# Optimization experiments

Measured on AMD Instinct MI355X. Metric: run time of the kernel, lower is better.

## Reference

```python
import jax, jax.numpy as jnp
import numpy as np
from functools import partial

B, C, H, W = 64, 3, 64, 64
D = 64            # hidden_dim == slot dim
S = 7             # num_slots
ITERS = 3
EPS_ATTN = 1e-8
MLP_HID = 128     # max(dim, 128)


def conv5_same(x, w, b):
    # x: [B, Cin, H, W], w: [Cout, Cin, 5, 5]
    y = jax.lax.conv_general_dilated(
        x, w, window_strides=(1, 1), padding='SAME',
        dimension_numbers=('NCHW', 'OIHW', 'NCHW'))
    return y + b[None, :, None, None]


def layernorm(x, w, b, eps):
    mu = jnp.mean(x, axis=-1, keepdims=True)
    var = jnp.var(x, axis=-1, keepdims=True)
    return (x - mu) * jax.lax.rsqrt(var + eps) * w + b


def build_grid(h, w):
    rr = jnp.linspace(0.0, 1.0, h)
    cc = jnp.linspace(0.0, 1.0, w)
    g = jnp.stack(jnp.meshgrid(rr, cc, indexing='ij'), axis=-1)  # [H,W,2]
    return jnp.concatenate([g, 1.0 - g], axis=-1)                # [H,W,4]


def setup_inputs() -> dict:
    key = jax.random.key(0)
    ks = jax.random.split(key, 32)
    sc = lambda fan: 1.0 / np.sqrt(fan)
    inp = {
        'image': jax.random.normal(ks[0], (B, C, H, W), jnp.float32),
        'slots_noise': jax.random.normal(ks[1], (B, S, D), jnp.float32),
        'conv0_w': jax.random.normal(ks[2], (D, 3, 5, 5), jnp.float32) * sc(3 * 25),
        'conv0_b': jnp.zeros((D,), jnp.float32),
        'conv1_w': jax.random.normal(ks[3], (D, D, 5, 5), jnp.float32) * sc(D * 25),
        'conv1_b': jnp.zeros((D,), jnp.float32),
        'conv2_w': jax.random.normal(ks[4], (D, D, 5, 5), jnp.float32) * sc(D * 25),
        'conv2_b': jnp.zeros((D,), jnp.float32),
        'conv3_w': jax.random.normal(ks[5], (D, D, 5, 5), jnp.float32) * sc(D * 25),
        'conv3_b': jnp.zeros((D,), jnp.float32),
        'pos_w': jax.random.normal(ks[6], (D, 4), jnp.float32) * sc(4),
        'pos_b': jnp.zeros((D,), jnp.float32),
        'fc1_w': jax.random.normal(ks[7], (D, D), jnp.float32) * sc(D),
        'fc1_b': jnp.zeros((D,), jnp.float32),
        'fc2_w': jax.random.normal(ks[8], (D, D), jnp.float32) * sc(D),
        'fc2_b': jnp.zeros((D,), jnp.float32),
        'slots_mu': jax.random.uniform(ks[9], (1, 1, D), jnp.float32, -0.3, 0.3),
        'slots_log_sigma': jax.random.uniform(ks[10], (1, 1, D), jnp.float32, -0.3, 0.3),
        'q_w': jax.random.normal(ks[11], (D, D), jnp.float32) * sc(D),
        'k_w': jax.random.normal(ks[12], (D, D), jnp.float32) * sc(D),
        'v_w': jax.random.normal(ks[13], (D, D), jnp.float32) * sc(D),
        'gru_w_ih': jax.random.normal(ks[14], (3 * D, D), jnp.float32) * sc(D),
        'gru_w_hh': jax.random.normal(ks[15], (3 * D, D), jnp.float32) * sc(D),
        'gru_b_ih': jnp.zeros((3 * D,), jnp.float32),
        'gru_b_hh': jnp.zeros((3 * D,), jnp.float32),
        'mlp1_w': jax.random.normal(ks[16], (MLP_HID, D), jnp.float32) * sc(D),
        'mlp1_b': jnp.zeros((MLP_HID,), jnp.float32),
        'mlp2_w': jax.random.normal(ks[17], (D, MLP_HID), jnp.float32) * sc(MLP_HID),
        'mlp2_b': jnp.zeros((D,), jnp.float32),
        'ln_in_w': jnp.ones((D,), jnp.float32),
        'ln_in_b': jnp.zeros((D,), jnp.float32),
        'ln_slots_w': jnp.ones((D,), jnp.float32),
        'ln_slots_b': jnp.zeros((D,), jnp.float32),
        'ln_ff_w': jnp.ones((D,), jnp.float32),
        'ln_ff_b': jnp.zeros((D,), jnp.float32),
    }
    return inp


def reference(image, slots_noise, conv0_w, conv0_b, conv1_w, conv1_b,
              conv2_w, conv2_b, conv3_w, conv3_b, pos_w, pos_b,
              fc1_w, fc1_b, fc2_w, fc2_b, slots_mu, slots_log_sigma,
              q_w, k_w, v_w, gru_w_ih, gru_w_hh, gru_b_ih, gru_b_hh,
              mlp1_w, mlp1_b, mlp2_w, mlp2_b,
              ln_in_w, ln_in_b, ln_slots_w, ln_slots_b, ln_ff_w, ln_ff_b):
    b = image.shape[0]
    # --- CNN encoder ---
    x = jax.nn.relu(conv5_same(image, conv0_w, conv0_b))
    x = jax.nn.relu(conv5_same(x, conv1_w, conv1_b))
    x = jax.nn.relu(conv5_same(x, conv2_w, conv2_b))
    x = jax.nn.relu(conv5_same(x, conv3_w, conv3_b))
    x = jnp.transpose(x, (0, 2, 3, 1))                 # [B,H,W,D]
    pos = build_grid(x.shape[1], x.shape[2]) @ pos_w.T + pos_b
    x = x + pos[None]
    x = x.reshape(b, -1, D)                            # [B,N,D]
    # LayerNorm over (N, D) jointly, fresh affine (w=1, b=0), eps=1e-5
    mu = jnp.mean(x, axis=(1, 2), keepdims=True)
    var = jnp.var(x, axis=(1, 2), keepdims=True)
    x = (x - mu) * jax.lax.rsqrt(var + 1e-5)
    # --- fc MLP ---
    x = jax.nn.relu(x @ fc1_w.T + fc1_b) @ fc2_w.T + fc2_b
    # --- Slot attention ---
    scale = D ** (-0.5)
    slots = slots_mu + jnp.exp(slots_log_sigma) * slots_noise  # [B,S,D]
    inp = layernorm(x, ln_in_w, ln_in_b, 1e-3)
    k = inp @ k_w.T                                    # [B,N,D]
    v = inp @ v_w.T
    for _ in range(ITERS):
        slots_prev = slots
        q = layernorm(slots, ln_slots_w, ln_slots_b, 1e-3) @ q_w.T  # [B,S,D]
        dots = jnp.einsum('bid,bjd->bij', q, k) * scale             # [B,S,N]
        attn = jax.nn.softmax(dots, axis=1) + EPS_ATTN              # over slots
        attn = attn / jnp.sum(attn, axis=-1, keepdims=True)
        updates = jnp.einsum('bjd,bij->bid', v, attn)               # [B,S,D]
        # GRUCell(updates, slots_prev)
        gi = updates @ gru_w_ih.T + gru_b_ih                        # [B,S,3D]
        gh = slots_prev @ gru_w_hh.T + gru_b_hh
        i_r, i_z, i_n = jnp.split(gi, 3, axis=-1)
        h_r, h_z, h_n = jnp.split(gh, 3, axis=-1)
        r = jax.nn.sigmoid(i_r + h_r)
        z = jax.nn.sigmoid(i_z + h_z)
        n = jnp.tanh(i_n + r * h_n)
        slots = (1.0 - z) * n + z * slots_prev
        # residual MLP
        h = layernorm(slots, ln_ff_w, ln_ff_b, 1e-3)
        slots = slots + (jax.nn.relu(h @ mlp1_w.T + mlp1_b) @ mlp2_w.T + mlp2_b)
    return slots
```

## Files before the change

### kernel.cpp

```cpp
#include <hip/hip_runtime.h>

#define HW 64
#define BATCH 64
#define DDIM 64
#define NSLOT 7
#define NPOS 4096

typedef __attribute__((ext_vector_type(8))) short short8;
typedef __attribute__((ext_vector_type(4))) short short4v;
typedef __attribute__((ext_vector_type(4))) float floatx4;

__device__ __forceinline__ float wave_sum(float x) {
  #pragma unroll
  for (int o = 32; o >= 1; o >>= 1) x += __shfl_xor(x, o, 64);
  return x;
}

__device__ __forceinline__ unsigned short f2bf(float f) {
  unsigned int u = __float_as_uint(f);
  return (unsigned short)((u + 0x7fffu + ((u >> 16) & 1u)) >> 16);
}
__device__ __forceinline__ float bf2f(unsigned short u) {
  return __uint_as_float(((unsigned int)u) << 16);
}
__device__ __forceinline__ short4v pack4(float a, float b, float c, float d) {
  short4v s;
  s.x = (short)f2bf(a); s.y = (short)f2bf(b);
  s.z = (short)f2bf(c); s.w = (short)f2bf(d);
  return s;
}

__global__ __launch_bounds__(256) void prep_w(
    const float* __restrict__ w1, const float* __restrict__ w2,
    const float* __restrict__ w3, unsigned short* __restrict__ wp)
{
  int idx = blockIdx.x * 256 + threadIdx.x;
  if (idx >= 3 * 102400) return;
  int L = idx / 102400;
  int rem = idx - L * 102400;
  int tap = rem >> 12;
  int r2  = rem & 4095;
  int ks = r2 >> 11;
  int mt = (r2 >> 9) & 3;
  int l  = (r2 >> 3) & 63;
  int j  = r2 & 7;
  int oc  = mt * 16 + (l & 15);
  int cin = (ks * 4 + (l >> 4)) * 8 + j;
  const float* w = (L == 0) ? w1 : (L == 1) ? w2 : w3;
  wp[idx] = f2bf(w[(oc * 64 + cin) * 25 + tap]);
}

__global__ __launch_bounds__(256) void prep_fcw(
    const float* __restrict__ f1, const float* __restrict__ f2,
    const float* __restrict__ kw, const float* __restrict__ vw,
    unsigned short* __restrict__ dst)
{
  int idx = blockIdx.x * 256 + threadIdx.x;
  int mat = idx >> 12;
  int r = idx & 4095;
  int ks = r >> 11;
  int mt = (r >> 9) & 3;
  int l  = (r >> 3) & 63;
  int j  = r & 7;
  int oc = mt * 16 + (l & 15);
  int in = (ks * 4 + (l >> 4)) * 8 + j;
  const float* src = (mat == 0) ? f1 : (mat == 1) ? f2 : (mat == 2) ? kw : vw;
  dst[idx] = f2bf(src[oc * 64 + in]);
}

__global__ void prep_s1(const float* __restrict__ f1, float* __restrict__ s1)
{
  int oc = threadIdx.x;
  float s = 0.f;
  for (int k = 0; k < 64; k++) s += f1[oc * 64 + k];
  s1[oc] = s;
}

__global__ __launch_bounds__(256) void conv0_relu(
    const float* __restrict__ in, const float* __restrict__ wgt,
    const float* __restrict__ bias, unsigned short* __restrict__ out)
{
  constexpr int TH = 8, TW = 32, OCT = 16, CIN = 3;
  __shared__ __align__(16) float sIn[CIN][TH + 4][40];
  __shared__ __align__(16) float sW[CIN][25][OCT];

  const int bx = blockIdx.x;
  const int tx = bx & 1;
  const int ty = (bx >> 1) & 7;
  const int b  = bx >> 4;
  const int ocb = blockIdx.y * OCT;
  const int x0 = tx * TW, y0 = ty * TH;
  const int tid = threadIdx.x;

  const int sq  = tid & 63;
  const int ocq = tid >> 6;
  const int yy  = sq >> 3;
  const int xx4 = (sq & 7) << 2;
  const int oc0 = ocq << 2;

  float acc[4][4];
  #pragma unroll
  for (int o = 0; o < 4; o++)
    #pragma unroll
    for (int x = 0; x < 4; x++) acc[o][x] = 0.f;

  for (int idx = tid; idx < CIN * 12 * 36; idx += 256) {
    int c  = idx % 36;
    int r  = (idx / 36) % 12;
    int ci = idx / (36 * 12);
    int gy = y0 - 2 + r, gx = x0 - 2 + c;
    float v = 0.f;
    if (gy >= 0 && gy < HW && gx >= 0 && gx < HW)
      v = in[((b * CIN + ci) * HW + gy) * HW + gx];
    sIn[ci][r][c] = v;
  }
  for (int idx = tid; idx < CIN * 25 * OCT; idx += 256) {
    int oc  = idx & 15;
    int tap = (idx >> 4) % 25;
    int ci  = idx / (16 * 25);
    sW[ci][tap][oc] = wgt[((ocb + oc) * CIN + ci) * 25 + tap];
  }
  __syncthreads();

  for (int ci = 0; ci < CIN; ci++) {
    #pragma unroll
    for (int dy = 0; dy < 5; dy++) {
      const float* rp = &sIn[ci][yy + dy][xx4];
      float4 a0 = *(const float4*)rp;
      float4 a1 = *(const float4*)(rp + 4);
      float vals[8] = {a0.x, a0.y, a0.z, a0.w, a1.x, a1.y, a1.z, a1.w};
      #pragma unroll
      for (int dx = 0; dx < 5; dx++) {
        float4 wv = *(const float4*)&sW[ci][dy * 5 + dx][oc0];
        float wa[4] = {wv.x, wv.y, wv.z, wv.w};
        #pragma unroll
        for (int o = 0; o < 4; o++)
          #pragma unroll
          for (int x = 0; x < 4; x++)
            acc[o][x] += wa[o] * vals[dx + x];
      }
    }
  }

  float bb[4];
  #pragma unroll
  for (int o = 0; o < 4; o++) bb[o] = bias[ocb + oc0 + o];
  #pragma unroll
  for (int x = 0; x < 4; x++) {
    int pos = (b << 12) + (y0 + yy) * 64 + (x0 + xx4 + x);
    *(short4v*)&out[pos * 64 + ocb + oc0] =
        pack4(fmaxf(acc[0][x] + bb[0], 0.f), fmaxf(acc[1][x] + bb[1], 0.f),
              fmaxf(acc[2][x] + bb[2], 0.f), fmaxf(acc[3][x] + bb[3], 0.f));
  }
}

template<int FUSE_POS>
__global__ __launch_bounds__(256) void conv_mfma(
    const unsigned short* __restrict__ in, const unsigned short* __restrict__ wp,
    const float* __restrict__ bias, unsigned short* __restrict__ out,
    const float* __restrict__ pos_w, const float* __restrict__ pos_b,
    float* __restrict__ stats)
{
  extern __shared__ short lds[];
  short* sIn = lds;
  uint4* sWu0 = (uint4*)(lds + 25600);
  uint4* sWu1 = sWu0 + 512;

  const int tid = threadIdx.x;
  const int b   = blockIdx.x >> 4;
  const int tile = blockIdx.x & 15;
  const int y0 = (tile >> 2) * 16, x0 = (tile & 3) * 16;

  const uint4* in4 = (const uint4*)in;
  for (int idx = tid; idx < 3200; idx += 256) {
    int p = idx >> 3, c = idx & 7;
    int py = p / 20, px = p - py * 20;
    int gy = y0 - 2 + py, gx = x0 - 2 + px;
    uint4 v = {0u, 0u, 0u, 0u};
    if ((unsigned)gy < 64u && (unsigned)gx < 64u)
      v = in4[(((b << 12) + (gy << 6) + gx) << 3) + c];
    *(uint4*)&sIn[(p << 6) + ((c ^ (p & 7)) << 3)] = v;
  }
  const uint4* wg = (const uint4*)wp;
  sWu0[tid] = wg[tid];
  sWu0[256 + tid] = wg[256 + tid];
  uint4 r0 = wg[512 + tid];
  uint4 r1 = wg[512 + 256 + tid];
  __syncthreads();

  const int w  = tid >> 6;
  const int l  = tid & 63;
  const int lx = l & 15;
  const int kq = l >> 4;
  const int w4 = w * 4;

  floatx4 zero4 = {0.f, 0.f, 0.f, 0.f};
  floatx4 acc[4][4];
  #pragma unroll
  for (int yy = 0; yy < 4; yy++)
    #pragma unroll
    for (int mt = 0; mt < 4; mt++) acc[yy][mt] = zero4;

  int dy = 0, dx = 0;
  #pragma unroll 1
  for (int t = 0; t < 25; ++t) {
    uint4* cur = (t & 1) ? sWu1 : sWu0;
    if (t < 24) {
      uint4* alt = (t & 1) ? sWu0 : sWu1;
      alt[tid] = r0;
      alt[256 + tid] = r1;
    }
    if (t < 23) {
      r0 = wg[(t + 2) * 512 + tid];
      r1 = wg[(t + 2) * 512 + 256 + tid];
    }
    const int ix = lx + dx;
    #pragma unroll
    for (int ks = 0; ks < 2; ++ks) {
      const int kc = ks * 4 + kq;
      short8 Bf[4];
      #pragma unroll
      for (int yy = 0; yy < 4; ++yy) {
        int p = (w4 + yy + dy) * 20 + ix;
        Bf[yy] = *(const short8*)&sIn[(p << 6) + ((kc ^ (p & 7)) << 3)];
      }
      #pragma unroll
      for (int mt = 0; mt < 4; ++mt) {
        uint4 Af4 = cur[(ks * 4 + mt) * 64 + l];
        #pragma unroll
        for (int yy = 0; yy < 4; ++yy)
          acc[yy][mt] = __builtin_amdgcn_mfma_f32_16x16x32_bf16(
              *(const short8*)&Af4, Bf[yy], acc[yy][mt], 0, 0, 0);
      }
    }
    if (t < 24) __syncthreads();
    if (++dx == 5) { dx = 0; ++dy; }
  }

  float4 bv[4];
  #pragma unroll
  for (int mt = 0; mt < 4; ++mt) bv[mt] = *(const float4*)&bias[mt * 16 + kq * 4];

  float4 pw[4][4];  float pb[4][4];
  if (FUSE_POS) {
    #pragma unroll
    for (int mt = 0; mt < 4; ++mt)
      #pragma unroll
      for (int r = 0; r < 4; ++r) {
        int d = mt * 16 + kq * 4 + r;
        pw[mt][r] = *(const float4*)&pos_w[d * 4];
        pb[mt][r] = pos_b[d];
      }
  }

  const int x = x0 + lx;
  const float cx = x * (1.0f / 63.0f);
  float lsum = 0.f, lsq = 0.f;

  #pragma unroll
  for (int yy = 0; yy < 4; ++yy) {
    const int y = y0 + w4 + yy;
    const float ry = y * (1.0f / 63.0f);
    const int base = ((b << 12) + y * 64 + x) * 64;
    #pragma unroll
    for (int mt = 0; mt < 4; ++mt) {
      float v[4];
      #pragma unroll
      for (int r = 0; r < 4; ++r) {
        float f = fmaxf(acc[yy][mt][r] + bv[mt][r], 0.f);
        if (FUSE_POS) {
          f += ry * pw[mt][r].x + cx * pw[mt][r].y + (1.f - ry) * pw[mt][r].z +
               (1.f - cx) * pw[mt][r].w + pb[mt][r];
          lsum += f; lsq += f * f;
        }
        v[r] = f;
      }
      *(short4v*)&out[base + mt * 16 + kq * 4] = pack4(v[0], v[1], v[2], v[3]);
    }
  }

  if (FUSE_POS) {
    lsum = wave_sum(lsum);
    lsq  = wave_sum(lsq);
    if (l == 0) {
      atomicAdd(&stats[b * 2], lsum);
      atomicAdd(&stats[b * 2 + 1], lsq);
    }
  }
}

__global__ void finalize_stats(const float* __restrict__ stats, float* __restrict__ ms)
{
  int b = threadIdx.x;
  float s = stats[b * 2], q = stats[b * 2 + 1];
  float mean = s * (1.0f / 262144.f);
  float var  = q * (1.0f / 262144.f) - mean * mean;
  ms[b * 2] = mean;
  ms[b * 2 + 1] = rsqrtf(var + 1e-5f);
}

__global__ __launch_bounds__(256) void fc_mfma(
    const unsigned short* __restrict__ xb, const float* __restrict__ ms,
    const unsigned short* __restrict__ wall, const float* __restrict__ fc1_b,
    const float* __restrict__ s1, const float* __restrict__ fc2_b,
    const float* __restrict__ ln_w, const float* __restrict__ ln_b,
    unsigned short* __restrict__ kb, unsigned short* __restrict__ vT)
{
  __shared__ short sA[64 * 64];
  __shared__ uint4 sW[2048];
  const int tid = threadIdx.x;
  const int w = tid >> 6, l = tid & 63, lx = l & 15, kq = l >> 4;
  const int p0 = blockIdx.x * 64;
  const int b  = blockIdx.x >> 6;
  const int posb = (blockIdx.x & 63) * 64;
  const int w16 = w * 16;
  const float mean = ms[b * 2], rstd = ms[b * 2 + 1];
  const float rmu = rstd * mean;

  const uint4* wg = (const uint4*)wall;
  #pragma unroll
  for (int i = 0; i < 8; ++i) sW[i * 256 + tid] = wg[i * 256 + tid];

  {
    const uint4* x4 = (const uint4*)xb;
    int r0 = w16 + (l >> 3), c = l & 7;
    uint4 v0 = x4[((p0 + r0) << 3) + c];
    uint4 v1 = x4[((p0 + r0 + 8) << 3) + c];
    *(uint4*)&sA[(r0 << 6) + ((c ^ (r0 & 7)) << 3)] = v0;
    int r1 = r0 + 8;
    *(uint4*)&sA[(r1 << 6) + ((c ^ (r1 & 7)) << 3)] = v1;
  }
  __syncthreads();

  const int brow = w16 + lx;
  floatx4 zero4 = {0.f, 0.f, 0.f, 0.f};

  #define GEMM64(MATI, ACC)                                                   \
    {                                                                         \
      _Pragma("unroll")                                                       \
      for (int ks = 0; ks < 2; ++ks) {                                        \
        int ch = (ks * 4 + kq) ^ (brow & 7);                                  \
        short8 Bf = *(const short8*)&sA[(brow << 6) + (ch << 3)];             \
        _Pragma("unroll")                                                     \
        for (int mt = 0; mt < 4; ++mt) {                                      \
          uint4 Af = sW[(MATI) * 512 + (ks * 4 + mt) * 64 + l];               \
          ACC[mt] = __builtin_amdgcn_mfma_f32_16x16x32_bf16(                  \
              *(const short8*)&Af, Bf, ACC[mt], 0, 0, 0);                     \
        }                                                                     \
      }                                                                       \
    }

  #define LDSW(MT, SV)                                                        \
    {                                                                         \
      int ch = ((MT) * 2 + (kq >> 1)) ^ (brow & 7);                           \
      *(short4v*)&sA[(brow << 6) + (ch << 3) + ((kq & 1) << 2)] = (SV);       \
    }

  floatx4 a1[4] = {zero4, zero4, zero4, zero4};
  GEMM64(0, a1);
  #pragma unroll
  for (int mt = 0; mt < 4; ++mt) {
    float4 b1v = *(const float4*)&fc1_b[mt * 16 + kq * 4];
    float4 s1v = *(const float4*)&s1[mt * 16 + kq * 4];
    float v[4];
    v[0] = fmaxf(rstd * a1[mt][0] - rmu * s1v.x + b1v.x, 0.f);
    v[1] = fmaxf(rstd * a1[mt][1] - rmu * s1v.y + b1v.y, 0.f);
    v[2] = fmaxf(rstd * a1[mt][2] - rmu * s1v.z + b1v.z, 0.f);
    v[3] = fmaxf(rstd * a1[mt][3] - rmu * s1v.w + b1v.w, 0.f);
    LDSW(mt, pack4(v[0], v[1], v[2], v[3]));
  }

  floatx4 a2[4] = {zero4, zero4, zero4, zero4};
  GEMM64(1, a2);
  float y2[4][4];
  float ps = 0.f, pq = 0.f;
  #pragma unroll
  for (int mt = 0; mt < 4; ++mt) {
    float4 b2v = *(const float4*)&fc2_b[mt * 16 + kq * 4];
    float bb[4] = {b2v.x, b2v.y, b2v.z, b2v.w};
    #pragma unroll
    for (int r = 0; r < 4; ++r) {
      float y = a2[mt][r] + bb[r];
      y2[mt][r] = y;
      ps += y; pq += y * y;
    }
  }
  ps += __shfl_xor(ps, 16, 64);  ps += __shfl_xor(ps, 32, 64);
  pq += __shfl_xor(pq, 16, 64);  pq += __shfl_xor(pq, 32, 64);
  float mu2 = ps * (1.f / 64.f);
  float rs2 = rsqrtf(pq * (1.f / 64.f) - mu2 * mu2 + 1e-3f);
  #pragma unroll
  for (int mt = 0; mt < 4; ++mt) {
    float4 lwv = *(const float4*)&ln_w[mt * 16 + kq * 4];
    float4 lbv = *(const float4*)&ln_b[mt * 16 + kq * 4];
    float v[4];
    v[0] = (y2[mt][0] - mu2) * rs2 * lwv.x + lbv.x;
    v[1] = (y2[mt][1] - mu2) * rs2 * lwv.y + lbv.y;
    v[2] = (y2[mt][2] - mu2) * rs2 * lwv.z + lbv.z;
    v[3] = (y2[mt][3] - mu2) * rs2 * lwv.w + lbv.w;
    LDSW(mt, pack4(v[0], v[1], v[2], v[3]));
  }

  floatx4 a3[4] = {zero4, zero4, zero4, zero4};
  GEMM64(2, a3);
  const int gbase = ((p0 + brow) << 6) + kq * 4;
  #pragma unroll
  for (int mt = 0; mt < 4; ++mt)
    *(short4v*)&kb[gbase + mt * 16] = pack4(a3[mt][0], a3[mt][1], a3[mt][2], a3[mt][3]);

  floatx4 a4[4] = {zero4, zero4, zero4, zero4};
  GEMM64(3, a4);
  #pragma unroll
  for (int mt = 0; mt < 4; ++mt)
    #pragma unroll
    for (int r = 0; r < 4; ++r)
      vT[((b << 6) + mt * 16 + kq * 4 + r) * 4096 + posb + brow] = f2bf(a4[mt][r]);

  #undef GEMM64
  #undef LDSW
}

__global__ __launch_bounds__(256) void slots_init(
    const float* __restrict__ mu, const float* __restrict__ ls,
    const float* __restrict__ noise, float* __restrict__ slots)
{
  int idx = blockIdx.x * 256 + threadIdx.x;
  if (idx < BATCH * NSLOT * DDIM) {
    int d = idx & 63;
    slots[idx] = mu[d] + expf(ls[d]) * noise[idx];
  }
}

__global__ __launch_bounds__(256) void attn_fused(
    const float* __restrict__ slots, const float* __restrict__ lnw,
    const float* __restrict__ lnb, const float* __restrict__ q_w,
    const unsigned short* __restrict__ kb, const unsigned short* __restrict__ vT,
    float* __restrict__ Upart, float* __restrict__ Tpart)
{
  __shared__ short sLN[7 * 64];
  __shared__ short sQ[16 * 64];
  __shared__ short sP[4][16 * 72];
  __shared__ float sUr[4][7 * 64];
  __shared__ float sT[4][8];
  const int b  = blockIdx.x >> 4;
  const int jt = blockIdx.x & 15;
  const int tid = threadIdx.x;
  const int w = tid >> 6, l = tid & 63, lx = l & 15, kq = l >> 4;
  floatx4 zero4 = {0.f, 0.f, 0.f, 0.f};

  for (int i = tid; i < 1024; i += 256) sQ[i] = 0;

  for (int s = w; s < 7; s += 4) {
    float v = slots[(b * 7 + s) * 64 + l];
    float m = wave_sum(v) * (1.f / 64.f);
    float dv = v - m;
    float var = wave_sum(dv * dv) * (1.f / 64.f);
    sLN[s * 64 + l] = (short)f2bf(dv * rsqrtf(var + 1e-3f) * lnw[l] + lnb[l]);
  }
  for (int s = w; s < 7; s += 4) {
    float acc = 0.f;
    #pragma unroll
    for (int e = 0; e < 64; e += 4) {
      float4 w4v = *(const float4*)&q_w[l * 64 + e];
      acc += w4v.x * bf2f(sLN[s * 64 + e])     + w4v.y * bf2f(sLN[s * 64 + e + 1])
           + w4v.z * bf2f(sLN[s * 64 + e + 2]) + w4v.w * bf2f(sLN[s * 64 + e + 3]);
    }
    sQ[s * 64 + l] = (short)f2bf(acc);
  }
  __syncthreads();

  uint4 qA[2];
  #pragma unroll
  for (int ks = 0; ks < 2; ++ks)
    qA[ks] = *(const uint4*)&sQ[lx * 64 + (ks * 4 + kq) * 8];

  const uint4* kb4 = (const uint4*)kb;
  const int row0 = kq * 4;
  const int j0 = jt * 256 + w * 64;
  float tacc[4] = {0.f, 0.f, 0.f, 0.f};
  short* sPw = sP[w];

  #pragma unroll
  for (int jh = 0; jh < 4; ++jh) {
    const int j = j0 + jh * 16 + lx;
    floatx4 d4 = zero4;
    #pragma unroll
    for (int ks = 0; ks < 2; ++ks) {
      uint4 kB = kb4[(((b << 12) + j) << 3) + ks * 4 + kq];
      d4 = __builtin_amdgcn_mfma_f32_16x16x32_bf16(
          *(const short8*)&qA[ks], *(const short8*)&kB, d4, 0, 0, 0);
    }
    float e[4];
    float mx = -1e30f;
    #pragma unroll
    for (int r = 0; r < 4; ++r) {
      e[r] = (row0 + r < 7) ? d4[r] * 0.125f : -1e30f;
      mx = fmaxf(mx, e[r]);
    }
    mx = fmaxf(mx, __shfl_xor(mx, 16, 64));
    mx = fmaxf(mx, __shfl_xor(mx, 32, 64));
    float sum = 0.f;
    #pragma unroll
    for (int r = 0; r < 4; ++r) {
      e[r] = (row0 + r < 7) ? __expf(e[r] - mx) : 0.f;
      sum += e[r];
    }
    sum += __shfl_xor(sum, 16, 64);
    sum += __shfl_xor(sum, 32, 64);
    float inv = 1.f / sum;
    #pragma unroll
    for (int r = 0; r < 4; ++r) {
      float p = (row0 + r < 7) ? e[r] * inv + 1e-8f : 0.f;
      tacc[r] += p;
      sPw[(row0 + r) * 72 + jh * 16 + lx] = (short)f2bf(p);
    }
  }

  #pragma unroll
  for (int r = 0; r < 4; ++r) {
    if (row0 + r < 7) {
      float t = tacc[r];
      t += __shfl_xor(t, 1, 64);  t += __shfl_xor(t, 2, 64);
      t += __shfl_xor(t, 4, 64);  t += __shfl_xor(t, 8, 64);
      if (lx == 0) sT[w][row0 + r] = t;
    }
  }
  __syncthreads();

  floatx4 uacc[4] = {zero4, zero4, zero4, zero4};
  #pragma unroll
  for (int nt = 0; nt < 4; ++nt) {
    #pragma unroll
    for (int ks = 0; ks < 2; ++ks) {
      short8 pa = *(const short8*)&sPw[lx * 72 + ks * 32 + kq * 8];
      uint4 vB = *(const uint4*)&vT[((b << 6) + nt * 16 + lx) * 4096 +
                                    j0 + ks * 32 + kq * 8];
      uacc[nt] = __builtin_amdgcn_mfma_f32_16x16x32_bf16(
          pa, *(const short8*)&vB, uacc[nt], 0, 0, 0);
    }
  }

  #pragma unroll
  for (int nt = 0; nt < 4; ++nt)
    #pragma unroll
    for (int r = 0; r < 4; ++r)
      if (row0 + r < 7)
        sUr[w][(row0 + r) * 64 + nt * 16 + lx] = uacc[nt][r];
  __syncthreads();

  const int slab = b * 16 + jt;
  for (int i = tid; i < 448; i += 256)
    Upart[slab * 448 + i] = sUr[0][i] + sUr[1][i] + sUr[2][i] + sUr[3][i];
  if (tid < 7)
    Tpart[slab * 7 + tid] = sT[0][tid] + sT[1][tid] + sT[2][tid] + sT[3][tid];
}

__global__ __launch_bounds__(192) void gru_mlp(
    const float* __restrict__ Upart, const float* __restrict__ Tpart,
    const float* __restrict__ w_ih, const float* __restrict__ w_hh,
    const float* __restrict__ b_ih, const float* __restrict__ b_hh,
    const float* __restrict__ lnfw, const float* __restrict__ lnfb,
    const float* __restrict__ m1w, const float* __restrict__ m1b,
    const float* __restrict__ m2w, const float* __restrict__ m2b,
    float* __restrict__ slots)
{
  __shared__ float sU[64], sSp[64], sGi[192], sGh[192], sH[64], sLn[64], sHid[128];
  const int bs = blockIdx.x;
  const int b = bs / 7, s = bs - b * 7;
  const int t = threadIdx.x;

  if (t < 64) {
    float u = 0.f, Ts = 0.f;
    #pragma unroll 4
    for (int jt = 0; jt < 16; ++jt) {
      u  += Upart[(b * 16 + jt) * 448 + s * 64 + t];
      Ts += Tpart[(b * 16 + jt) * 7 + s];
    }
    sU[t] = u / Ts;
    sSp[t] = slots[bs * 64 + t];
  }
  __syncthreads();
  {
    float gi = b_ih[t], gh = b_hh[t];
    #pragma unroll
    for (int d = 0; d < 64; d += 4) {
      float4 wi = *(const float4*)&w_ih[t * 64 + d];
      float4 wh = *(const float4*)&w_hh[t * 64 + d];
      gi += wi.x * sU[d] + wi.y * sU[d + 1] + wi.z * sU[d + 2] + wi.w * sU[d + 3];
      gh += wh.x * sSp[d] + wh.y * sSp[d + 1] + wh.z * sSp[d + 2] + wh.w * sSp[d + 3];
    }
    sGi[t] = gi; sGh[t] = gh;
  }
  __syncthreads();
  if (t < 64) {
    float r = 1.f / (1.f + expf(-(sGi[t] + sGh[t])));
    float z = 1.f / (1.f + expf(-(sGi[64 + t] + sGh[64 + t])));
    float n = tanhf(sGi[128 + t] + r * sGh[128 + t]);
    float h = (1.f - z) * n + z * sSp[t];
    sH[t] = h;
    float m = wave_sum(h) * (1.f / 64.f);
    float dv = h - m;
    float var = wave_sum(dv * dv) * (1.f / 64.f);
    sLn[t] = dv * rsqrtf(var + 1e-3f) * lnfw[t] + lnfb[t];
  }
  __syncthreads();
  if (t < 128) {
    float a = m1b[t];
    #pragma unroll
    for (int d = 0; d < 64; d += 4) {
      float4 w = *(const float4*)&m1w[t * 64 + d];
      a += w.x * sLn[d] + w.y * sLn[d + 1] + w.z * sLn[d + 2] + w.w * sLn[d + 3];
    }
    sHid[t] = fmaxf(a, 0.f);
  }
  __syncthreads();
  if (t < 64) {
    float a = m2b[t];
    #pragma unroll
    for (int k = 0; k < 128; k += 4) {
      float4 w = *(const float4*)&m2w[t * 128 + k];
      a += w.x * sHid[k] + w.y * sHid[k + 1] + w.z * sHid[k + 2] + w.w * sHid[k + 3];
    }
    slots[bs * 64 + t] = sH[t] + a;
  }
}

extern "C" void kernel_launch(void* const* d_in, const int* in_sizes, int n_in,
                              void* d_out, int out_size, void* d_ws, size_t ws_size,
                              hipStream_t stream)
{
  const float* image    = (const float*)d_in[0];
  const float* noise    = (const float*)d_in[1];
  const float* conv0_w  = (const float*)d_in[2];
  const float* conv0_b  = (const float*)d_in[3];
  const float* conv1_w  = (const float*)d_in[4];
  const float* conv1_b  = (const float*)d_in[5];
  const float* conv2_w  = (const float*)d_in[6];
  const float* conv2_b  = (const float*)d_in[7];
  const float* conv3_w  = (const float*)d_in[8];
  const float* conv3_b  = (const float*)d_in[9];
  const float* pos_w    = (const float*)d_in[10];
  const float* pos_b    = (const float*)d_in[11];
  const float* fc1_w    = (const float*)d_in[12];
  const float* fc1_b    = (const float*)d_in[13];
  const float* fc2_w    = (const float*)d_in[14];
  const float* fc2_b    = (const float*)d_in[15];
  const float* slots_mu = (const float*)d_in[16];
  const float* slots_ls = (const float*)d_in[17];
  const float* q_w      = (const float*)d_in[18];
  const float* k_w      = (const float*)d_in[19];
  const float* v_w      = (const float*)d_in[20];
  const float* gru_w_ih = (const float*)d_in[21];
  const float* gru_w_hh = (const float*)d_in[22];
  const float* gru_b_ih = (const float*)d_in[23];
  const float* gru_b_hh = (const float*)d_in[24];
  const float* mlp1_w   = (const float*)d_in[25];
  const float* mlp1_b   = (const float*)d_in[26];
  const float* mlp2_w   = (const float*)d_in[27];
  const float* mlp2_b   = (const float*)d_in[28];
  const float* ln_in_w  = (const float*)d_in[29];
  const float* ln_in_b  = (const float*)d_in[30];
  const float* ln_sl_w  = (const float*)d_in[31];
  const float* ln_sl_b  = (const float*)d_in[32];
  const float* ln_ff_w  = (const float*)d_in[33];
  const float* ln_ff_b  = (const float*)d_in[34];

  float* ws = (float*)d_ws;
  float* R1   = ws;
  float* R2   = R1 + 16777216;
  float* Pbuf = R2 + 16777216;
  float* qbuf  = Pbuf + 1835008;
  float* slots = qbuf + 28672;
  float* Ubuf  = slots + 28672;
  float* Tbuf  = Ubuf + 28672;
  float* stats = Tbuf + 448;
  float* ms    = stats + 128;

  unsigned short* Wp  = (unsigned short*)Pbuf;
  unsigned short* wfc = Wp + 307200;
  float* s1f = (float*)(wfc + 16384);
  float* Upart = Pbuf + 262144;
  float* Tpart = Upart + 458752;
  unsigned short* Y0 = (unsigned short*)R1;
  unsigned short* Y1 = (unsigned short*)R2;
  unsigned short* xb = (unsigned short*)R2;
  unsigned short* kb = (unsigned short*)R1;
  unsigned short* vT = kb + 16777216;

  prep_w<<<1200, 256, 0, stream>>>(conv1_w, conv2_w, conv3_w, Wp);
  prep_fcw<<<64, 256, 0, stream>>>(fc1_w, fc2_w, k_w, v_w, wfc);
  prep_s1<<<1, 64, 0, stream>>>(fc1_w, s1f);
  hipMemsetAsync(stats, 0, 128 * sizeof(float), stream);

  dim3 cgrid(1024, 4);
  conv0_relu<<<cgrid, 256, 0, stream>>>(image, conv0_w, conv0_b, Y0);
  conv_mfma<0><<<1024, 256, 67584, stream>>>(Y0, Wp,          conv1_b, Y1,
                                             nullptr, nullptr, nullptr);
  conv_mfma<0><<<1024, 256, 67584, stream>>>(Y1, Wp + 102400, conv2_b, Y0,
                                             nullptr, nullptr, nullptr);
  conv_mfma<1><<<1024, 256, 67584, stream>>>(Y0, Wp + 204800, conv3_b, xb,
                                             pos_w, pos_b, stats);
  finalize_stats<<<1, 64, 0, stream>>>(stats, ms);

  fc_mfma<<<4096, 256, 0, stream>>>(xb, ms, wfc, fc1_b, s1f, fc2_b,
                                    ln_in_w, ln_in_b, kb, vT);

  slots_init<<<112, 256, 0, stream>>>(slots_mu, slots_ls, noise, slots);

  for (int it = 0; it < 3; it++) {
    attn_fused<<<1024, 256, 0, stream>>>(slots, ln_sl_w, ln_sl_b, q_w,
                                         kb, vT, Upart, Tpart);
    gru_mlp<<<448, 192, 0, stream>>>(Upart, Tpart, gru_w_ih, gru_w_hh,
                                     gru_b_ih, gru_b_hh, ln_ff_w, ln_ff_b,
                                     mlp1_w, mlp1_b, mlp2_w, mlp2_b, slots);
  }

  hipMemcpyAsync(d_out, slots, 28672 * sizeof(float), hipMemcpyDeviceToDevice, stream);
}
```

Measured before the change: 499.1 us.

## Split conv input channels into two chunks to halve LDS and raise occupancy

The 5x5 MFMA conv now processes input channels in two chunks of 32. Each chunk stages only half the halo tile (padded 40-short row stride) and half the weight slices in LDS, which cuts shared memory from about 66KB to about 39KB per block. Launch bounds request 4 blocks per CU to exploit this. In exchange the input tile is reloaded per chunk, there are twice as many synchronised tap iterations with half the MFMA work each, and the tighter register budget may cause spills.

Result: slower. 518.5 us (+3.9%).

```diff
diff --git a/kernel.cpp b/kernel.cpp
--- a/kernel.cpp
+++ b/kernel.cpp
@@ -155,7 +155,7 @@
 }
 
 template<int FUSE_POS>
-__global__ __launch_bounds__(256) void conv_mfma(
+__global__ __launch_bounds__(256, 4) void conv_mfma(
     const unsigned short* __restrict__ in, const unsigned short* __restrict__ wp,
     const float* __restrict__ bias, unsigned short* __restrict__ out,
     const float* __restrict__ pos_w, const float* __restrict__ pos_b,
@@ -163,30 +163,13 @@
 {
   extern __shared__ short lds[];
   short* sIn = lds;
-  uint4* sWu0 = (uint4*)(lds + 25600);
-  uint4* sWu1 = sWu0 + 512;
+  uint4* sWu0 = (uint4*)(lds + 16000);
+  uint4* sWu1 = sWu0 + 256;
 
   const int tid = threadIdx.x;
   const int b   = blockIdx.x >> 4;
   const int tile = blockIdx.x & 15;
   const int y0 = (tile >> 2) * 16, x0 = (tile & 3) * 16;
-
-  const uint4* in4 = (const uint4*)in;
-  for (int idx = tid; idx < 3200; idx += 256) {
-    int p = idx >> 3, c = idx & 7;
-    int py = p / 20, px = p - py * 20;
-    int gy = y0 - 2 + py, gx = x0 - 2 + px;
-    uint4 v = {0u, 0u, 0u, 0u};
-    if ((unsigned)gy < 64u && (unsigned)gx < 64u)
-      v = in4[(((b << 12) + (gy << 6) + gx) << 3) + c];
-    *(uint4*)&sIn[(p << 6) + ((c ^ (p & 7)) << 3)] = v;
-  }
-  const uint4* wg = (const uint4*)wp;
-  sWu0[tid] = wg[tid];
-  sWu0[256 + tid] = wg[256 + tid];
-  uint4 r0 = wg[512 + tid];
-  uint4 r1 = wg[512 + 256 + tid];
-  __syncthreads();
 
   const int w  = tid >> 6;
   const int l  = tid & 63;
@@ -201,40 +184,54 @@
     #pragma unroll
     for (int mt = 0; mt < 4; mt++) acc[yy][mt] = zero4;
 
-  int dy = 0, dx = 0;
+  const uint4* in4 = (const uint4*)in;
+  const uint4* wg = (const uint4*)wp;
+
   #pragma unroll 1
-  for (int t = 0; t < 25; ++t) {
-    uint4* cur = (t & 1) ? sWu1 : sWu0;
-    if (t < 24) {
-      uint4* alt = (t & 1) ? sWu0 : sWu1;
-      alt[tid] = r0;
-      alt[256 + tid] = r1;
-    }
-    if (t < 23) {
-      r0 = wg[(t + 2) * 512 + tid];
-      r1 = wg[(t + 2) * 512 + 256 + tid];
-    }
-    const int ix = lx + dx;
-    #pragma unroll
-    for (int ks = 0; ks < 2; ++ks) {
-      const int kc = ks * 4 + kq;
+  for (int chunk = 0; chunk < 2; ++chunk) {
+    __syncthreads();
+    for (int idx = tid; idx < 1600; idx += 256) {
+      int p = idx >> 2, u = idx & 3;
+      int py = p / 20, px = p - py * 20;
+      int gy = y0 - 2 + py, gx = x0 - 2 + px;
+      uint4 v = {0u, 0u, 0u, 0u};
+      if ((unsigned)gy < 64u && (unsigned)gx < 64u)
+        v = in4[(((b << 12) + (gy << 6) + gx) << 3) + chunk * 4 + u];
+      *(uint4*)&sIn[p * 40 + ((u ^ (p & 3)) << 3)] = v;
+    }
+    const int base = chunk * 256;
+    sWu0[tid] = wg[base + tid];
+    uint4 r0 = wg[base + 512 + tid];
+    __syncthreads();
+
+    int dy = 0, dx = 0;
+    #pragma unroll 1
+    for (int t = 0; t < 25; ++t) {
+      uint4* cur = (t & 1) ? sWu1 : sWu0;
+      if (t < 24) {
+        uint4* alt = (t & 1) ? sWu0 : sWu1;
+        alt[tid] = r0;
+      }
+      if (t < 23)
+        r0 = wg[base + (t + 2) * 512 + tid];
+      const int ix = lx + dx;
       short8 Bf[4];
       #pragma unroll
       for (int yy = 0; yy < 4; ++yy) {
         int p = (w4 + yy + dy) * 20 + ix;
-        Bf[yy] = *(const short8*)&sIn[(p << 6) + ((kc ^ (p & 7)) << 3)];
+        Bf[yy] = *(const short8*)&sIn[p * 40 + ((kq ^ (p & 3)) << 3)];
       }
       #pragma unroll
       for (int mt = 0; mt < 4; ++mt) {
-        uint4 Af4 = cur[(ks * 4 + mt) * 64 + l];
+        uint4 Af4 = cur[mt * 64 + l];
         #pragma unroll
         for (int yy = 0; yy < 4; ++yy)
           acc[yy][mt] = __builtin_amdgcn_mfma_f32_16x16x32_bf16(
               *(const short8*)&Af4, Bf[yy], acc[yy][mt], 0, 0, 0);
       }
-    }
-    if (t < 24) __syncthreads();
-    if (++dx == 5) { dx = 0; ++dy; }
+      if (t < 24) __syncthreads();
+      if (++dx == 5) { dx = 0; ++dy; }
+    }
   }
 
   float4 bv[4];
@@ -694,11 +691,11 @@
 
   dim3 cgrid(1024, 4);
   conv0_relu<<<cgrid, 256, 0, stream>>>(image, conv0_w, conv0_b, Y0);
-  conv_mfma<0><<<1024, 256, 67584, stream>>>(Y0, Wp,          conv1_b, Y1,
+  conv_mfma<0><<<1024, 256, 40192, stream>>>(Y0, Wp,          conv1_b, Y1,
                                              nullptr, nullptr, nullptr);
-  conv_mfma<0><<<1024, 256, 67584, stream>>>(Y1, Wp + 102400, conv2_b, Y0,
+  conv_mfma<0><<<1024, 256, 40192, stream>>>(Y1, Wp + 102400, conv2_b, Y0,
                                              nullptr, nullptr, nullptr);
-  conv_mfma<1><<<1024, 256, 67584, stream>>>(Y0, Wp + 204800, conv3_b, xb,
+  conv_mfma<1><<<1024, 256, 40192, stream>>>(Y0, Wp + 204800, conv3_b, xb,
                                              pos_w, pos_b, stats);
   finalize_stats<<<1, 64, 0, stream>>>(stats, ms);
 
```
